# Optimization experiments

Hardware: AMD Instinct MI355X
Metric: run time of the kernel (lower is better)

## Reference

```python
import jax, jax.numpy as jnp
import numpy as np

N_NODES = 100000
N_EDGES = 1600000
HIDDEN = 128
N_FILTERS = 64
CUTOFF = 8.0
BN_EPS = 1e-3  # keras BatchNormalization default epsilon


def setup_inputs() -> dict:
    key = jax.random.key(0)
    ks = jax.random.split(key, 12)
    x = jax.random.normal(ks[0], (N_NODES, HIDDEN), dtype=jnp.float32)
    edge_index = jax.random.randint(ks[1], (2, N_EDGES), 0, N_NODES, dtype=jnp.int32)
    edge_weight = jax.random.uniform(ks[2], (N_EDGES,), dtype=jnp.float32) * CUTOFF
    edge_attr = jax.random.uniform(ks[3], (N_EDGES, 1), dtype=jnp.float32)
    s = 0.05
    # filter_net: Dense(1->64, tanh), Dense(64->64)
    Wf1 = jax.random.normal(ks[4], (1, N_FILTERS), dtype=jnp.float32) * s
    bf1 = jnp.zeros((N_FILTERS,), jnp.float32)
    Wf2 = jax.random.normal(ks[5], (N_FILTERS, N_FILTERS), dtype=jnp.float32) * s
    bf2 = jnp.zeros((N_FILTERS,), jnp.float32)
    # interaction_net: Dense(128->128, softplus), Dense(128->128)
    Wi1 = jax.random.normal(ks[6], (HIDDEN, HIDDEN), dtype=jnp.float32) * s
    bi1 = jnp.zeros((HIDDEN,), jnp.float32)
    Wi2 = jax.random.normal(ks[7], (HIDDEN, HIDDEN), dtype=jnp.float32) * s
    bi2 = jnp.zeros((HIDDEN,), jnp.float32)
    # BatchNormalization (inference: moving stats)
    gamma = jnp.ones((HIDDEN,), jnp.float32)
    beta = jnp.zeros((HIDDEN,), jnp.float32)
    mov_mean = jax.random.normal(ks[8], (HIDDEN,), dtype=jnp.float32) * 0.01
    mov_var = jnp.ones((HIDDEN,), jnp.float32)
    return {"x": x, "edge_index": edge_index, "edge_weight": edge_weight,
            "edge_attr": edge_attr, "Wf1": Wf1, "bf1": bf1, "Wf2": Wf2, "bf2": bf2,
            "Wi1": Wi1, "bi1": bi1, "Wi2": Wi2, "bi2": bi2,
            "gamma": gamma, "beta": beta, "mov_mean": mov_mean, "mov_var": mov_var}


def reference(x, edge_index, edge_weight, edge_attr, Wf1, bf1, Wf2, bf2,
              Wi1, bi1, Wi2, bi2, gamma, beta, mov_mean, mov_var):
    row, col = edge_index[0], edge_index[1]
    # continuous filters with smooth cosine cutoff
    scaled = edge_weight * (2.0 / CUTOFF) - 1.0                    # [E]
    h = jnp.tanh(scaled[:, None] @ Wf1 + bf1)                      # [E, F]
    filters = h @ Wf2 + bf2                                        # [E, F]
    cut = 0.5 * (jnp.cos(edge_weight * jnp.pi / CUTOFF) + 1.0)
    cut = jnp.where(edge_weight <= CUTOFF, cut, 0.0)               # [E]
    filters = filters * cut[:, None]
    # Original: (neighbor[:, None, :] * filters[:, :, None]).sum(axis=1)
    # == neighbor * filters.sum(-1, keepdims) — same math, no [E,F,H] tensor.
    fsum = jnp.sum(filters, axis=-1, keepdims=True)                # [E, 1]
    messages = x[col] * fsum                                       # [E, H]
    agg = jax.ops.segment_sum(messages, row, num_segments=x.shape[0])  # [N, H]
    out = jax.nn.softplus(agg @ Wi1 + bi1) @ Wi2 + bi2             # [N, H]
    # BatchNormalization, inference mode (training=False)
    out = gamma * (out - mov_mean) * jax.lax.rsqrt(mov_var + BN_EPS) + beta
    return out
```

## Files before the change

kernel.cpp:

```cpp
#include <hip/hip_runtime.h>
#include <math.h>

#define HIDDEN 128
#define NFILT 64
#define SCAN_B 1024
#define LUTK 2048

typedef __attribute__((ext_vector_type(8))) short bf16x8;
typedef __attribute__((ext_vector_type(4))) float f32x4;
typedef __attribute__((ext_vector_type(4))) float f32x4v;
typedef __attribute__((ext_vector_type(2))) int i32x2;

__device__ __forceinline__ short f2bf(float f) {
    unsigned u = __float_as_uint(f);
    unsigned r = (u + 0x7fffu + ((u >> 16) & 1u)) >> 16;
    return (short)r;
}
__device__ __forceinline__ float bf2f(unsigned short u) {
    return __uint_as_float(((unsigned)u) << 16);
}

__device__ __forceinline__ float softplus_fast(float v) {
    float e = __builtin_amdgcn_exp2f(v * 1.4426950408889634f);
    float r = 0.69314718055994531f * __builtin_amdgcn_logf(1.0f + e);
    return (v > 80.f) ? v : r;
}

__global__ void wsum_kernel(const float* __restrict__ Wf2, const float* __restrict__ bf2,
                            float* __restrict__ wsum, float* __restrict__ bsum) {
    int j = threadIdx.x;
    float s = 0.f;
    for (int f = 0; f < NFILT; ++f) s += Wf2[j * NFILT + f];
    wsum[j] = s;
    if (j == 0) {
        float b = 0.f;
        for (int f = 0; f < NFILT; ++f) b += bf2[f];
        *bsum = b;
    }
}

__device__ __forceinline__ float edge_coeff(float w,
                                            const float* sW, const float* sB,
                                            const float* sS, float bsum) {
    float s = fmaf(w, 0.25f, -1.0f);
    float acc = bsum;
    #pragma unroll 8
    for (int j = 0; j < NFILT; ++j)
        acc += tanhf(fmaf(s, sW[j], sB[j])) * sS[j];
    float cut = (w <= 8.0f) ? 0.5f * (cosf(w * 0.39269908169872414f) + 1.0f) : 0.0f;
    return acc * cut;
}

__global__ void lut_kernel(const float* __restrict__ Wf1, const float* __restrict__ bf1,
                           const float* __restrict__ wsum, const float* __restrict__ bsum,
                           float* __restrict__ lut) {
    int i = blockIdx.x * 256 + threadIdx.x;
    if (i > LUTK) return;
    float w = 8.0f * (float)i / (float)LUTK;
    lut[i] = edge_coeff(w, Wf1, bf1, wsum, *bsum);
}

__device__ __forceinline__ float lut_eval(const float* sl, float w) {
    float t = w * ((float)LUTK / 8.0f);
    t = fminf(fmaxf(t, 0.f), (float)LUTK);
    int i = (int)t;
    i = min(i, LUTK - 1);
    return fmaf(t - (float)i, sl[i + 1] - sl[i], sl[i]);
}

__global__ void prep_w_kernel(const float* __restrict__ Wi1, const float* __restrict__ Wi2,
                              short* __restrict__ W1T, short* __restrict__ W2T,
                              const float* __restrict__ Wf2, const float* __restrict__ bf2,
                              float* __restrict__ wsum, float* __restrict__ bsum,
                              const float* __restrict__ bi2,
                              const float* __restrict__ gamma, const float* __restrict__ beta,
                              const float* __restrict__ mean, const float* __restrict__ var,
                              float* __restrict__ scf, float* __restrict__ shf,
                              int* __restrict__ zbuf, int zn) {
    int idx = blockIdx.x * 256 + threadIdx.x;
    const float* src = (idx < 16384) ? Wi1 : Wi2;
    short* dst = (idx < 16384) ? W1T : W2T;
    int i = idx & 16383;
    int k = i >> 7, n = i & 127;
    dst[n * HIDDEN + k] = f2bf(src[i]);

    for (int z = idx; z * 4 < zn; z += 32768) {
        if (z * 4 + 3 < zn) *(int4*)&zbuf[z * 4] = make_int4(0, 0, 0, 0);
        else for (int q = z * 4; q < zn; ++q) zbuf[q] = 0;
    }

    if (blockIdx.x == 0 && threadIdx.x < 64) {
        int j = threadIdx.x;
        float s = 0.f;
        for (int f = 0; f < NFILT; ++f) s += Wf2[j * NFILT + f];
        wsum[j] = s;
        if (j == 0) {
            float b = 0.f;
            for (int f = 0; f < NFILT; ++f) b += bf2[f];
            *bsum = b;
        }
    }
    if (blockIdx.x == 1 && threadIdx.x < HIDDEN) {
        int j = threadIdx.x;
        float sc = gamma[j] * rsqrtf(var[j] + 1e-3f);
        scf[j] = sc;
        shf[j] = (bi2[j] - mean[j]) * sc + beta[j];
    }
}

__global__ __launch_bounds__(256) void x2q_count_kernel(
    const float* __restrict__ x, signed char* __restrict__ xq,
    float* __restrict__ xscale, int N16,
    const int* __restrict__ rows, int* __restrict__ deg,
    int* __restrict__ rank, int E) {
    int i = blockIdx.x * 256 + threadIdx.x;
    if (i < E) rank[i] = atomicAdd(&deg[rows[i]], 1);
    if (i < N16) {
        int node = i >> 4, lane = i & 15;
        const float* xp = &x[(size_t)node * HIDDEN + lane * 8];
        const f32x4v v0 = __builtin_nontemporal_load((const f32x4v*)xp);
        const f32x4v v1 = __builtin_nontemporal_load((const f32x4v*)(xp + 4));
        float v[8] = {v0[0], v0[1], v0[2], v0[3], v1[0], v1[1], v1[2], v1[3]};
        float m = 0.f;
        #pragma unroll
        for (int j = 0; j < 8; ++j) m = fmaxf(m, fabsf(v[j]));
        #pragma unroll
        for (int off = 8; off > 0; off >>= 1)
            m = fmaxf(m, __shfl_xor(m, off, 16));
        float si = (m > 0.f) ? 127.f / m : 0.f;
        int q[8];
        #pragma unroll
        for (int j = 0; j < 8; ++j) q[j] = __float2int_rn(v[j] * si);
        int lo = (q[0] & 0xff) | ((q[1] & 0xff) << 8) |
                 ((q[2] & 0xff) << 16) | ((q[3] & 0xff) << 24);
        int hi = (q[4] & 0xff) | ((q[5] & 0xff) << 8) |
                 ((q[6] & 0xff) << 16) | ((q[7] & 0xff) << 24);
        *(int2*)&xq[(size_t)node * HIDDEN + lane * 8] = make_int2(lo, hi);
        if (lane == 0) xscale[node] = m * (1.f / 127.f);
    }
}

__global__ void count_rank_kernel(const int* __restrict__ rows, int* __restrict__ deg,
                                  int* __restrict__ rank, int E) {
    int e = blockIdx.x * blockDim.x + threadIdx.x;
    if (e < E) rank[e] = atomicAdd(&deg[rows[e]], 1);
}

__global__ void count_kernel(const int* __restrict__ rows, int* __restrict__ deg, int E) {
    int e = blockIdx.x * blockDim.x + threadIdx.x;
    if (e < E) atomicAdd(&deg[rows[e]], 1);
}

__global__ __launch_bounds__(SCAN_B) void scan_p1(const int* __restrict__ deg,
                                                  int* __restrict__ bsums, int N) {
    __shared__ int red[SCAN_B];
    int i = blockIdx.x * SCAN_B + threadIdx.x;
    red[threadIdx.x] = (i < N) ? deg[i] : 0;
    __syncthreads();
    for (int off = SCAN_B / 2; off > 0; off >>= 1) {
        if (threadIdx.x < off) red[threadIdx.x] += red[threadIdx.x + off];
        __syncthreads();
    }
    if (threadIdx.x == 0) bsums[blockIdx.x] = red[0];
}

__global__ __launch_bounds__(SCAN_B) void scan_p2(int* __restrict__ bsums, int B) {
    __shared__ int part[SCAN_B];
    int t = threadIdx.x;
    part[t] = (t < B) ? bsums[t] : 0;
    __syncthreads();
    for (int off = 1; off < SCAN_B; off <<= 1) {
        int v = (t >= off) ? part[t - off] : 0;
        __syncthreads();
        part[t] += v;
        __syncthreads();
    }
    if (t < B) bsums[t] = (t == 0) ? 0 : part[t - 1];
}

template <bool WRITE_CURSOR>
__global__ __launch_bounds__(SCAN_B) void scan_p3_t(int* __restrict__ deg,
                                                    const int* __restrict__ bsums,
                                                    int* __restrict__ offs, int N) {
    __shared__ int part[SCAN_B];
    int t = threadIdx.x;
    int i = blockIdx.x * SCAN_B + t;
    int d = (i < N) ? deg[i] : 0;
    part[t] = d;
    __syncthreads();
    for (int off = 1; off < SCAN_B; off <<= 1) {
        int v = (t >= off) ? part[t - off] : 0;
        __syncthreads();
        part[t] += v;
        __syncthreads();
    }
    int pre = bsums[blockIdx.x] + part[t] - d;
    if (i < N) {
        offs[i] = pre;
        if (WRITE_CURSOR) deg[i] = pre;
        if (i == N - 1) offs[N] = pre + d;
    }
}

__global__ __launch_bounds__(256) void fill_rank_q_kernel(
    const int* __restrict__ rows, const int* __restrict__ cols,
    const float* __restrict__ ew, const int* __restrict__ rank,
    const int* __restrict__ offs, const float* __restrict__ xscale,
    const float* __restrict__ lut, int2* __restrict__ epack, int E) {
    __shared__ float sl[LUTK + 1];
    for (int i = threadIdx.x; i <= LUTK; i += 256) sl[i] = lut[i];
    __syncthreads();
    int e = blockIdx.x * 256 + threadIdx.x;
    if (e >= E) return;
    float f = lut_eval(sl, __builtin_nontemporal_load(&ew[e]));
    int r = __builtin_nontemporal_load(&rows[e]);
    int c = __builtin_nontemporal_load(&cols[e]);
    float fs = f * xscale[c];
    int pos = offs[r] + __builtin_nontemporal_load(&rank[e]);
    epack[pos] = make_int2(c, __float_as_int(fs));
}

__global__ __launch_bounds__(256) void fill_rank_kernel(
    const int* __restrict__ rows, const int* __restrict__ cols,
    const float* __restrict__ ew, const int* __restrict__ rank,
    const int* __restrict__ offs, const float* __restrict__ lut,
    int2* __restrict__ epack, int E) {
    __shared__ float sl[LUTK + 1];
    for (int i = threadIdx.x; i <= LUTK; i += 256) sl[i] = lut[i];
    __syncthreads();
    int e = blockIdx.x * 256 + threadIdx.x;
    if (e >= E) return;
    float f = lut_eval(sl, __builtin_nontemporal_load(&ew[e]));
    int pos = offs[__builtin_nontemporal_load(&rows[e])] +
              __builtin_nontemporal_load(&rank[e]);
    epack[pos] = make_int2(__builtin_nontemporal_load(&cols[e]), __float_as_int(f));
}

__global__ __launch_bounds__(256) void fill_cursor_kernel(
    const int* __restrict__ rows, const int* __restrict__ cols,
    const float* __restrict__ ew, int* __restrict__ cursor,
    const float* __restrict__ lut, int2* __restrict__ epack, int E) {
    __shared__ float sl[LUTK + 1];
    for (int i = threadIdx.x; i <= LUTK; i += 256) sl[i] = lut[i];
    __syncthreads();
    int e = blockIdx.x * 256 + threadIdx.x;
    if (e >= E) return;
    float f = lut_eval(sl, ew[e]);
    int pos = atomicAdd(&cursor[rows[e]], 1);
    epack[pos] = make_int2(cols[e], __float_as_int(f));
}

__device__ __forceinline__ void qfma8(int lo, int hi, float f, float* a) {
    a[0] = fmaf((float)((int)(((unsigned)lo) << 24) >> 24), f, a[0]);
    a[1] = fmaf((float)((int)(((unsigned)lo) << 16) >> 24), f, a[1]);
    a[2] = fmaf((float)((int)(((unsigned)lo) << 8) >> 24), f, a[2]);
    a[3] = fmaf((float)(lo >> 24), f, a[3]);
    a[4] = fmaf((float)((int)(((unsigned)hi) << 24) >> 24), f, a[4]);
    a[5] = fmaf((float)((int)(((unsigned)hi) << 16) >> 24), f, a[5]);
    a[6] = fmaf((float)((int)(((unsigned)hi) << 8) >> 24), f, a[6]);
    a[7] = fmaf((float)(hi >> 24), f, a[7]);
}

__device__ __forceinline__ void qfma16(int4 q, float f, float* a) {
    qfma8(q.x, q.y, f, a);
    qfma8(q.z, q.w, f, a + 8);
}

__global__ __launch_bounds__(256) void gather_q8_kernel(const int* __restrict__ offs,
                                                        const int2* __restrict__ epack,
                                                        const signed char* __restrict__ xq,
                                                        short* __restrict__ aggh, int N) {
    int t = threadIdx.x;
    int node = blockIdx.x * 32 + (t >> 3);
    if (node >= N) return;
    int lane = t & 7;
    int s = offs[node], eend = offs[node + 1];
    const signed char* xb = xq + lane * 16;

    float a[16];
    #pragma unroll
    for (int j = 0; j < 16; ++j) a[j] = 0.f;

    int i = s;
    for (; i + 4 <= eend; i += 4) {
        i32x2 p0 = __builtin_nontemporal_load((const i32x2*)&epack[i]);
        i32x2 p1 = __builtin_nontemporal_load((const i32x2*)&epack[i + 1]);
        i32x2 p2 = __builtin_nontemporal_load((const i32x2*)&epack[i + 2]);
        i32x2 p3 = __builtin_nontemporal_load((const i32x2*)&epack[i + 3]);
        int4 q0 = *(const int4*)(xb + (size_t)p0[0] * HIDDEN);
        int4 q1 = *(const int4*)(xb + (size_t)p1[0] * HIDDEN);
        int4 q2 = *(const int4*)(xb + (size_t)p2[0] * HIDDEN);
        int4 q3 = *(const int4*)(xb + (size_t)p3[0] * HIDDEN);
        qfma16(q0, __int_as_float(p0[1]), a);
        qfma16(q1, __int_as_float(p1[1]), a);
        qfma16(q2, __int_as_float(p2[1]), a);
        qfma16(q3, __int_as_float(p3[1]), a);
    }
    for (; i < eend; ++i) {
        i32x2 p = __builtin_nontemporal_load((const i32x2*)&epack[i]);
        int4 q = *(const int4*)(xb + (size_t)p[0] * HIDDEN);
        qfma16(q, __int_as_float(p[1]), a);
    }

    bf16x8 o0, o1;
    #pragma unroll
    for (int j = 0; j < 8; ++j) { o0[j] = f2bf(a[j]); o1[j] = f2bf(a[j + 8]); }
    short* op = &aggh[(size_t)node * HIDDEN + lane * 16];
    *(bf16x8*)op = o0;
    *(bf16x8*)(op + 8) = o1;
}

__global__ __launch_bounds__(256) void gather_kernel(const int* __restrict__ offs,
                                                     const int2* __restrict__ epack,
                                                     const float* __restrict__ x,
                                                     float* __restrict__ agg, int N) {
    int t = threadIdx.x;
    int node = blockIdx.x * 8 + (t >> 5);
    if (node >= N) return;
    int lane = t & 31;
    int s = offs[node], eend = offs[node + 1];
    float4 acc = make_float4(0.f, 0.f, 0.f, 0.f);
    int i = s;
    for (; i + 2 <= eend; i += 2) {
        int2 p0 = epack[i];
        int2 p1 = epack[i + 1];
        float4 x0 = *(const float4*)&x[(size_t)p0.x * HIDDEN + lane * 4];
        float4 x1 = *(const float4*)&x[(size_t)p1.x * HIDDEN + lane * 4];
        float f0 = __int_as_float(p0.y), f1 = __int_as_float(p1.y);
        acc.x = fmaf(x0.x, f0, acc.x); acc.y = fmaf(x0.y, f0, acc.y);
        acc.z = fmaf(x0.z, f0, acc.z); acc.w = fmaf(x0.w, f0, acc.w);
        acc.x = fmaf(x1.x, f1, acc.x); acc.y = fmaf(x1.y, f1, acc.y);
        acc.z = fmaf(x1.z, f1, acc.z); acc.w = fmaf(x1.w, f1, acc.w);
    }
    for (; i < eend; ++i) {
        int2 p = epack[i];
        float f = __int_as_float(p.y);
        const float4 xv = *(const float4*)&x[(size_t)p.x * HIDDEN + lane * 4];
        acc.x = fmaf(xv.x, f, acc.x);
        acc.y = fmaf(xv.y, f, acc.y);
        acc.z = fmaf(xv.z, f, acc.z);
        acc.w = fmaf(xv.w, f, acc.w);
    }
    *(float4*)&agg[(size_t)node * HIDDEN + lane * 4] = acc;
}

#define HROW 136

#define WSWZ(b) ((b) ^ ((((b) >> 8) & 7) << 4))

__global__ __launch_bounds__(512) void mlp_mfma_bf_kernel(
    const short* __restrict__ aggh, float* __restrict__ io,
    const short* __restrict__ W1T, const short* __restrict__ W2T,
    const float* __restrict__ bi1,
    const float* __restrict__ scf, const float* __restrict__ shf,
    int N) {
    __shared__ short wS[HIDDEN * HIDDEN];
    __shared__ short hS[128 * HROW];

    const int t = threadIdx.x;
    const int wave = t >> 6;
    const int lane = t & 63;
    const int quad = lane >> 4;
    const int m16  = lane & 15;
    const int row0 = blockIdx.x * 128 + wave * 16;
    const int arow = row0 + m16;

    const int swzmask = (m16 & 7) << 4;

    bf16x8 w2r[4];
    {
        const bf16x8* w1v = (const bf16x8*)W1T;
        const bf16x8* w2v = (const bf16x8*)W2T;
        bf16x8 w1r[4];
        #pragma unroll
        for (int j = 0; j < 4; ++j) w1r[j] = w1v[t + 512 * j];
        #pragma unroll
        for (int j = 0; j < 4; ++j) w2r[j] = w2v[t + 512 * j];
        #pragma unroll
        for (int j = 0; j < 4; ++j) {
            int b = (t + 512 * j) * 16;
            *(bf16x8*)((char*)wS + WSWZ(b)) = w1r[j];
        }
    }

    float b1v[8];
    #pragma unroll
    for (int ct = 0; ct < 8; ++ct) b1v[ct] = bi1[ct * 16 + m16];

    f32x4 acc[8];
    #pragma unroll
    for (int ct = 0; ct < 8; ++ct) acc[ct] = (f32x4)(0.f);

    __syncthreads();

    #pragma unroll
    for (int ks = 0; ks < 4; ++ks) {
        bf16x8 a;
        if (arow < N) {
            a = *(const bf16x8*)&aggh[(size_t)arow * HIDDEN + ks * 32 + quad * 8];
        } else {
            #pragma unroll
            for (int j = 0; j < 8; ++j) a[j] = 0;
        }
        const char* bbase = (const char*)wS + m16 * 256 + ((ks * 64 + quad * 16) ^ swzmask);
        #pragma unroll
        for (int ct = 0; ct < 8; ++ct) {
            bf16x8 b = *(const bf16x8*)(bbase + ct * 4096);
            acc[ct] = __builtin_amdgcn_mfma_f32_16x16x32_bf16(a, b, acc[ct], 0, 0, 0);
        }
    }

    #pragma unroll
    for (int ct = 0; ct < 8; ++ct) {
        int col = ct * 16 + m16;
        #pragma unroll
        for (int r = 0; r < 4; ++r) {
            int lrow = wave * 16 + quad * 4 + r;
            float h = softplus_fast(acc[ct][r] + b1v[ct]);
            hS[lrow * HROW + col] = f2bf(h);
        }
        acc[ct] = (f32x4)(0.f);
    }
    __syncthreads();

    #pragma unroll
    for (int j = 0; j < 4; ++j) {
        int b = (t + 512 * j) * 16;
        *(bf16x8*)((char*)wS + WSWZ(b)) = w2r[j];
    }
    __syncthreads();

    float scv[8], shv[8];
    #pragma unroll
    for (int ct = 0; ct < 8; ++ct) {
        scv[ct] = scf[ct * 16 + m16];
        shv[ct] = shf[ct * 16 + m16];
    }

    #pragma unroll
    for (int ks = 0; ks < 4; ++ks) {
        bf16x8 a = *(const bf16x8*)&hS[(wave * 16 + m16) * HROW + ks * 32 + quad * 8];
        const char* bbase = (const char*)wS + m16 * 256 + ((ks * 64 + quad * 16) ^ swzmask);
        #pragma unroll
        for (int ct = 0; ct < 8; ++ct) {
            bf16x8 b = *(const bf16x8*)(bbase + ct * 4096);
            acc[ct] = __builtin_amdgcn_mfma_f32_16x16x32_bf16(a, b, acc[ct], 0, 0, 0);
        }
    }

    #pragma unroll
    for (int r = 0; r < 4; ++r) {
        int grow = row0 + quad * 4 + r;
        if (grow < N) {
            float* p = &io[(size_t)grow * HIDDEN + m16];
            #pragma unroll
            for (int ct = 0; ct < 8; ++ct)
                __builtin_nontemporal_store(fmaf(acc[ct][r], scv[ct], shv[ct]), p + ct * 16);
        }
    }
}

__global__ __launch_bounds__(256) void mlp_mfma_kernel(
    float* io,
    const short* __restrict__ W1T, const short* __restrict__ W2T,
    const float* __restrict__ bi1,
    const float* __restrict__ scf, const float* __restrict__ shf,
    int N) {
    __shared__ short hS[64 * HROW];

    const int t = threadIdx.x;
    const int wave = t >> 6;
    const int lane = t & 63;
    const int quad = lane >> 4;
    const int m16  = lane & 15;
    const int row0 = blockIdx.x * 64 + wave * 16;
    const int arow = row0 + m16;

    f32x4 acc[8];
    #pragma unroll
    for (int ct = 0; ct < 8; ++ct) acc[ct] = (f32x4)(0.f);

    #pragma unroll
    for (int ks = 0; ks < 4; ++ks) {
        bf16x8 a;
        if (arow < N) {
            const float* ap = &io[(size_t)arow * HIDDEN + ks * 32 + quad * 8];
            float4 v0 = *(const float4*)ap;
            float4 v1 = *(const float4*)(ap + 4);
            a[0] = f2bf(v0.x); a[1] = f2bf(v0.y); a[2] = f2bf(v0.z); a[3] = f2bf(v0.w);
            a[4] = f2bf(v1.x); a[5] = f2bf(v1.y); a[6] = f2bf(v1.z); a[7] = f2bf(v1.w);
        } else {
            #pragma unroll
            for (int j = 0; j < 8; ++j) a[j] = 0;
        }
        #pragma unroll
        for (int ct = 0; ct < 8; ++ct) {
            bf16x8 b = *(const bf16x8*)&W1T[(ct * 16 + m16) * HIDDEN + ks * 32 + quad * 8];
            acc[ct] = __builtin_amdgcn_mfma_f32_16x16x32_bf16(a, b, acc[ct], 0, 0, 0);
        }
    }

    #pragma unroll
    for (int ct = 0; ct < 8; ++ct) {
        int col = ct * 16 + m16;
        float b1 = bi1[col];
        #pragma unroll
        for (int r = 0; r < 4; ++r) {
            int lrow = wave * 16 + quad * 4 + r;
            float h = softplus_fast(acc[ct][r] + b1);
            hS[lrow * HROW + col] = f2bf(h);
            acc[ct][r] = 0.f;
        }
    }
    __syncthreads();

    #pragma unroll
    for (int ks = 0; ks < 4; ++ks) {
        bf16x8 a = *(const bf16x8*)&hS[(wave * 16 + m16) * HROW + ks * 32 + quad * 8];
        #pragma unroll
        for (int ct = 0; ct < 8; ++ct) {
            bf16x8 b = *(const bf16x8*)&W2T[(ct * 16 + m16) * HIDDEN + ks * 32 + quad * 8];
            acc[ct] = __builtin_amdgcn_mfma_f32_16x16x32_bf16(a, b, acc[ct], 0, 0, 0);
        }
    }

    #pragma unroll
    for (int ct = 0; ct < 8; ++ct) {
        int col = ct * 16 + m16;
        float sc = scf[col], sh = shf[col];
        #pragma unroll
        for (int r = 0; r < 4; ++r) {
            int grow = row0 + quad * 4 + r;
            if (grow < N)
                io[(size_t)grow * HIDDEN + col] = fmaf(acc[ct][r], sc, sh);
        }
    }
}

__global__ void edge_filter_kernel(const float* __restrict__ ew,
                                   const float* __restrict__ Wf1, const float* __restrict__ bf1,
                                   const float* __restrict__ wsum, const float* __restrict__ bsum,
                                   float* __restrict__ fs, int E) {
    __shared__ float sW[NFILT], sB[NFILT], sS[NFILT];
    if (threadIdx.x < NFILT) {
        sW[threadIdx.x] = Wf1[threadIdx.x];
        sB[threadIdx.x] = bf1[threadIdx.x];
        sS[threadIdx.x] = wsum[threadIdx.x];
    }
    __syncthreads();
    int e = blockIdx.x * blockDim.x + threadIdx.x;
    if (e >= E) return;
    fs[e] = edge_coeff(ew[e], sW, sB, sS, *bsum);
}

__global__ void scatter_kernel(const int* __restrict__ rows, const int* __restrict__ cols,
                               const float* __restrict__ x, const float* __restrict__ fs,
                               float* __restrict__ agg, int E) {
    int t = threadIdx.x;
    int e = blockIdx.x * 8 + (t >> 5);
    if (e >= E) return;
    int lane = t & 31;
    int r = rows[e];
    int c = cols[e];
    float f = fs[e];
    const float4 xv = *(const float4*)&x[c * HIDDEN + lane * 4];
    float* dst = &agg[r * HIDDEN + lane * 4];
    atomicAdd(dst + 0, xv.x * f);
    atomicAdd(dst + 1, xv.y * f);
    atomicAdd(dst + 2, xv.z * f);
    atomicAdd(dst + 3, xv.w * f);
}

__global__ __launch_bounds__(256) void mlp_kernel(
    float* __restrict__ io,
    const float* __restrict__ Wi1, const float* __restrict__ bi1,
    const float* __restrict__ Wi2, const float* __restrict__ bi2,
    const float* __restrict__ gamma, const float* __restrict__ beta,
    const float* __restrict__ mean, const float* __restrict__ var,
    int N) {
    __shared__ float As[64 * HIDDEN];
    __shared__ float Wh[64 * HIDDEN];

    const int t = threadIdx.x;
    const int row0 = blockIdx.x * 64;
    const int col4 = (t & 31) * 4;
    const int rgrp = t >> 5;

    #pragma unroll
    for (int i = 0; i < 8; ++i) {
        int f4 = t + 256 * i;
        int r = f4 >> 5, c4 = (f4 & 31) * 4;
        int node = row0 + r;
        float4 v = make_float4(0.f, 0.f, 0.f, 0.f);
        if (node < N) v = *(const float4*)&io[node * HIDDEN + c4];
        *(float4*)&As[r * HIDDEN + c4] = v;
    }

    float acc[8][4];
    #pragma unroll
    for (int r = 0; r < 8; ++r)
        for (int j = 0; j < 4; ++j) acc[r][j] = 0.f;

    for (int kh = 0; kh < 2; ++kh) {
        __syncthreads();
        #pragma unroll
        for (int i = 0; i < 8; ++i) {
            int f4 = t + 256 * i;
            int kr = f4 >> 5, c4 = (f4 & 31) * 4;
            *(float4*)&Wh[kr * HIDDEN + c4] = *(const float4*)&Wi1[(kh * 64 + kr) * HIDDEN + c4];
        }
        __syncthreads();
        for (int k = 0; k < 64; ++k) {
            float4 w = *(const float4*)&Wh[k * HIDDEN + col4];
            #pragma unroll
            for (int r = 0; r < 8; ++r) {
                float a = As[(rgrp + 8 * r) * HIDDEN + kh * 64 + k];
                acc[r][0] = fmaf(a, w.x, acc[r][0]);
                acc[r][1] = fmaf(a, w.y, acc[r][1]);
                acc[r][2] = fmaf(a, w.z, acc[r][2]);
                acc[r][3] = fmaf(a, w.w, acc[r][3]);
            }
        }
    }
    __syncthreads();

    {
        float4 b = *(const float4*)&bi1[col4];
        float bv[4] = {b.x, b.y, b.z, b.w};
        #pragma unroll
        for (int r = 0; r < 8; ++r) {
            float hv[4];
            #pragma unroll
            for (int j = 0; j < 4; ++j) {
                float v = acc[r][j] + bv[j];
                hv[j] = softplus_fast(v);
                acc[r][j] = 0.f;
            }
            *(float4*)&As[(rgrp + 8 * r) * HIDDEN + col4] =
                make_float4(hv[0], hv[1], hv[2], hv[3]);
        }
    }

    for (int kh = 0; kh < 2; ++kh) {
        __syncthreads();
        #pragma unroll
        for (int i = 0; i < 8; ++i) {
            int f4 = t + 256 * i;
            int kr = f4 >> 5, c4 = (f4 & 31) * 4;
            *(float4*)&Wh[kr * HIDDEN + c4] = *(const float4*)&Wi2[(kh * 64 + kr) * HIDDEN + c4];
        }
        __syncthreads();
        for (int k = 0; k < 64; ++k) {
            float4 w = *(const float4*)&Wh[k * HIDDEN + col4];
            #pragma unroll
            for (int r = 0; r < 8; ++r) {
                float a = As[(rgrp + 8 * r) * HIDDEN + kh * 64 + k];
                acc[r][0] = fmaf(a, w.x, acc[r][0]);
                acc[r][1] = fmaf(a, w.y, acc[r][1]);
                acc[r][2] = fmaf(a, w.z, acc[r][2]);
                acc[r][3] = fmaf(a, w.w, acc[r][3]);
            }
        }
    }

    {
        float4 b2 = *(const float4*)&bi2[col4];
        float4 g  = *(const float4*)&gamma[col4];
        float4 be = *(const float4*)&beta[col4];
        float4 mu = *(const float4*)&mean[col4];
        float4 va = *(const float4*)&var[col4];
        float bv[4]  = {b2.x, b2.y, b2.z, b2.w};
        float gv[4]  = {g.x, g.y, g.z, g.w};
        float bev[4] = {be.x, be.y, be.z, be.w};
        float muv[4] = {mu.x, mu.y, mu.z, mu.w};
        float vav[4] = {va.x, va.y, va.z, va.w};
        float sc[4];
        #pragma unroll
        for (int j = 0; j < 4; ++j) sc[j] = gv[j] * rsqrtf(vav[j] + 1e-3f);
        #pragma unroll
        for (int r = 0; r < 8; ++r) {
            int node = row0 + rgrp + 8 * r;
            if (node < N) {
                float o[4];
                #pragma unroll
                for (int j = 0; j < 4; ++j)
                    o[j] = (acc[r][j] + bv[j] - muv[j]) * sc[j] + bev[j];
                *(float4*)&io[node * HIDDEN + col4] = make_float4(o[0], o[1], o[2], o[3]);
            }
        }
    }
}

extern "C" void kernel_launch(void* const* d_in, const int* in_sizes, int n_in,
                              void* d_out, int out_size, void* d_ws, size_t ws_size,
                              hipStream_t stream) {
    const float* x    = (const float*)d_in[0];
    const int*   ei   = (const int*)d_in[1];
    const float* ew   = (const float*)d_in[2];
    const float* Wf1  = (const float*)d_in[4];
    const float* bf1  = (const float*)d_in[5];
    const float* Wf2  = (const float*)d_in[6];
    const float* bf2  = (const float*)d_in[7];
    const float* Wi1  = (const float*)d_in[8];
    const float* bi1  = (const float*)d_in[9];
    const float* Wi2  = (const float*)d_in[10];
    const float* bi2  = (const float*)d_in[11];
    const float* gam  = (const float*)d_in[12];
    const float* bet  = (const float*)d_in[13];
    const float* mmu  = (const float*)d_in[14];
    const float* mva  = (const float*)d_in[15];

    const int N = in_sizes[0] / HIDDEN;
    const int E = in_sizes[2];
    const int* rows = ei;
    const int* cols = ei + E;

    float* io = (float*)d_out;

    const int B = (N + SCAN_B - 1) / SCAN_B;

    char* ws = (char*)d_ws;
    int*   deg    = (int*)ws;
    int*   offs   = deg + N;
    int*   bsums  = offs + N + 1;
    float* wsumv  = (float*)(bsums + B);
    float* bsumv  = wsumv + NFILT;
    float* lut    = bsumv + 1;
    size_t hdr_ints  = (size_t)(2 * N + 1 + B + NFILT + 1 + LUTK + 1);
    size_t epack_off = ((hdr_ints * 4) + 15) & ~(size_t)15;
    int2*  epack  = (int2*)(ws + epack_off);
    size_t wT_off = (epack_off + (size_t)E * sizeof(int2) + 15) & ~(size_t)15;
    short* W1T    = (short*)(ws + wT_off);
    short* W2T    = W1T + HIDDEN * HIDDEN;
    float* scf    = (float*)(W2T + HIDDEN * HIDDEN);
    float* shf    = scf + HIDDEN;
    size_t base_need = wT_off + 2 * HIDDEN * HIDDEN * sizeof(short) + 2 * HIDDEN * sizeof(float);
    size_t rank_off  = (base_need + 15) & ~(size_t)15;
    int*   rank   = (int*)(ws + rank_off);
    size_t rank_need = rank_off + (size_t)E * sizeof(int);
    size_t xq_off    = (rank_need + 15) & ~(size_t)15;
    signed char* xq  = (signed char*)(ws + xq_off);
    size_t xs_off    = (xq_off + (size_t)N * HIDDEN + 15) & ~(size_t)15;
    float* xscale    = (float*)(ws + xs_off);
    size_t ag_off    = (xs_off + (size_t)N * sizeof(float) + 15) & ~(size_t)15;
    short* aggh      = (short*)(ws + ag_off);
    size_t bf_need   = ag_off + (size_t)N * HIDDEN * sizeof(short);

    if (ws_size >= base_need && B <= SCAN_B) {
        const bool use_rank = (ws_size >= rank_need);
        const bool use_bf   = (ws_size >= bf_need);
        if (!use_bf) {
            hipMemsetAsync(deg, 0, (size_t)N * sizeof(int), stream);
        }
        prep_w_kernel<<<128, 256, 0, stream>>>(Wi1, Wi2, W1T, W2T,
                                               Wf2, bf2, wsumv, bsumv,
                                               bi2, gam, bet, mmu, mva, scf, shf,
                                               deg, use_bf ? N : 0);
        lut_kernel<<<(LUTK + 256) / 256, 256, 0, stream>>>(Wf1, bf1, wsumv, bsumv, lut);
        if (use_bf) {
            int N16 = N * 16;
            int work = (N16 > E) ? N16 : E;
            x2q_count_kernel<<<(work + 255) / 256, 256, 0, stream>>>(x, xq, xscale, N16,
                                                                     rows, deg, rank, E);
        } else if (use_rank) {
            count_rank_kernel<<<(E + 255) / 256, 256, 0, stream>>>(rows, deg, rank, E);
        } else {
            count_kernel<<<(E + 255) / 256, 256, 0, stream>>>(rows, deg, E);
        }
        scan_p1<<<B, SCAN_B, 0, stream>>>(deg, bsums, N);
        scan_p2<<<1, SCAN_B, 0, stream>>>(bsums, B);
        if (use_bf) {
            scan_p3_t<false><<<B, SCAN_B, 0, stream>>>(deg, bsums, offs, N);
            fill_rank_q_kernel<<<(E + 255) / 256, 256, 0, stream>>>(rows, cols, ew, rank,
                                                                    offs, xscale, lut,
                                                                    epack, E);
            gather_q8_kernel<<<(N + 31) / 32, 256, 0, stream>>>(offs, epack, xq, aggh, N);
            mlp_mfma_bf_kernel<<<(N + 127) / 128, 512, 0, stream>>>(aggh, io, W1T, W2T,
                                                                    bi1, scf, shf, N);
        } else if (use_rank) {
            scan_p3_t<false><<<B, SCAN_B, 0, stream>>>(deg, bsums, offs, N);
            fill_rank_kernel<<<(E + 255) / 256, 256, 0, stream>>>(rows, cols, ew, rank,
                                                                  offs, lut, epack, E);
            gather_kernel<<<(N + 7) / 8, 256, 0, stream>>>(offs, epack, x, io, N);
            mlp_mfma_kernel<<<(N + 63) / 64, 256, 0, stream>>>(io, W1T, W2T, bi1, scf, shf, N);
        } else {
            scan_p3_t<true><<<B, SCAN_B, 0, stream>>>(deg, bsums, offs, N);
            fill_cursor_kernel<<<(E + 255) / 256, 256, 0, stream>>>(rows, cols, ew, deg,
                                                                    lut, epack, E);
            gather_kernel<<<(N + 7) / 8, 256, 0, stream>>>(offs, epack, x, io, N);
            mlp_mfma_kernel<<<(N + 63) / 64, 256, 0, stream>>>(io, W1T, W2T, bi1, scf, shf, N);
        }
    } else {
        float* fs = (float*)d_ws;
        float* w2 = fs + E;
        float* b2 = w2 + NFILT;
        hipMemsetAsync(d_out, 0, (size_t)out_size * sizeof(float), stream);
        wsum_kernel<<<1, 64, 0, stream>>>(Wf2, bf2, w2, b2);
        edge_filter_kernel<<<(E + 255) / 256, 256, 0, stream>>>(ew, Wf1, bf1, w2, b2, fs, E);
        scatter_kernel<<<(E + 7) / 8, 256, 0, stream>>>(rows, cols, x, fs, io, E);
        mlp_kernel<<<(N + 63) / 64, 256, 0, stream>>>(io, Wi1, bi1, Wi2, bi2,
                                                      gam, bet, mmu, mva, N);
    }
}
```

Before: 342.2 us.

## Fuse count, scan and fill into one persistent kernel with grid barriers

Replaces the separate quantize/count, three-pass scan, and fill kernels with a single persistent kernel of 196 blocks that separates its phases with atomic-counter grid barriers. The LUT construction is folded into prep_w_kernel, which also zeroes the barrier counter. This removes several kernel launches and their inter-kernel gaps. In exchange it relies on all 196 blocks being co-resident for the spin barriers, and the grid-stride loops run at lower parallelism than the original launches.

```diff
diff --git a/kernel.cpp b/kernel.cpp
--- a/kernel.cpp
+++ b/kernel.cpp
@@ -5,6 +5,8 @@
 #define NFILT 64
 #define SCAN_B 1024
 #define LUTK 2048
+#define NBLK 196
+#define BBS  512
 
 typedef __attribute__((ext_vector_type(8))) short bf16x8;
 typedef __attribute__((ext_vector_type(4))) float f32x4;
@@ -24,6 +26,21 @@
     float e = __builtin_amdgcn_exp2f(v * 1.4426950408889634f);
     float r = 0.69314718055994531f * __builtin_amdgcn_logf(1.0f + e);
     return (v > 80.f) ? v : r;
+}
+
+__device__ __forceinline__ void gridbar(int* cnt, int phase) {
+    __syncthreads();
+    if (threadIdx.x == 0) {
+        __threadfence();
+        atomicAdd(cnt, 1);
+        int need = NBLK * phase;
+        while (__hip_atomic_load(cnt, __ATOMIC_ACQUIRE,
+                                 __HIP_MEMORY_SCOPE_AGENT) < need) {
+            __builtin_amdgcn_s_sleep(8);
+        }
+        __threadfence();
+    }
+    __syncthreads();
 }
 
 __global__ void wsum_kernel(const float* __restrict__ Wf2, const float* __restrict__ bf2,
@@ -51,15 +68,6 @@
     return acc * cut;
 }
 
-__global__ void lut_kernel(const float* __restrict__ Wf1, const float* __restrict__ bf1,
-                           const float* __restrict__ wsum, const float* __restrict__ bsum,
-                           float* __restrict__ lut) {
-    int i = blockIdx.x * 256 + threadIdx.x;
-    if (i > LUTK) return;
-    float w = 8.0f * (float)i / (float)LUTK;
-    lut[i] = edge_coeff(w, Wf1, bf1, wsum, *bsum);
-}
-
 __device__ __forceinline__ float lut_eval(const float* sl, float w) {
     float t = w * ((float)LUTK / 8.0f);
     t = fminf(fmaxf(t, 0.f), (float)LUTK);
@@ -76,7 +84,12 @@
                               const float* __restrict__ gamma, const float* __restrict__ beta,
                               const float* __restrict__ mean, const float* __restrict__ var,
                               float* __restrict__ scf, float* __restrict__ shf,
+                              const float* __restrict__ Wf1, const float* __restrict__ bf1,
+                              float* __restrict__ lut,
                               int* __restrict__ zbuf, int zn) {
+    __shared__ float sW[NFILT], sB[NFILT], sS[NFILT];
+    __shared__ float sbsum;
+
     int idx = blockIdx.x * 256 + threadIdx.x;
     const float* src = (idx < 16384) ? Wi1 : Wi2;
     short* dst = (idx < 16384) ? W1T : W2T;
@@ -106,37 +119,120 @@
         scf[j] = sc;
         shf[j] = (bi2[j] - mean[j]) * sc + beta[j];
     }
-}
-
-__global__ __launch_bounds__(256) void x2q_count_kernel(
+    if (blockIdx.x >= 2 && blockIdx.x <= 10) {
+        if (threadIdx.x < NFILT) {
+            int j = threadIdx.x;
+            float s = 0.f;
+            for (int f = 0; f < NFILT; ++f) s += Wf2[j * NFILT + f];
+            sS[j] = s;
+            sW[j] = Wf1[j];
+            sB[j] = bf1[j];
+        }
+        if (threadIdx.x == 0) {
+            float b = 0.f;
+            for (int f = 0; f < NFILT; ++f) b += bf2[f];
+            sbsum = b;
+        }
+        __syncthreads();
+        int li = (blockIdx.x - 2) * 256 + threadIdx.x;
+        if (li <= LUTK) {
+            float w = 8.0f * (float)li / (float)LUTK;
+            lut[li] = edge_coeff(w, sW, sB, sS, sbsum);
+        }
+    }
+}
+
+__global__ __launch_bounds__(BBS) void build_kernel(
     const float* __restrict__ x, signed char* __restrict__ xq,
-    float* __restrict__ xscale, int N16,
-    const int* __restrict__ rows, int* __restrict__ deg,
-    int* __restrict__ rank, int E) {
-    int i = blockIdx.x * 256 + threadIdx.x;
-    if (i < E) rank[i] = atomicAdd(&deg[rows[i]], 1);
-    if (i < N16) {
-        int node = i >> 4, lane = i & 15;
-        const float* xp = &x[(size_t)node * HIDDEN + lane * 8];
-        const f32x4v v0 = __builtin_nontemporal_load((const f32x4v*)xp);
-        const f32x4v v1 = __builtin_nontemporal_load((const f32x4v*)(xp + 4));
-        float v[8] = {v0[0], v0[1], v0[2], v0[3], v1[0], v1[1], v1[2], v1[3]};
-        float m = 0.f;
-        #pragma unroll
-        for (int j = 0; j < 8; ++j) m = fmaxf(m, fabsf(v[j]));
-        #pragma unroll
-        for (int off = 8; off > 0; off >>= 1)
-            m = fmaxf(m, __shfl_xor(m, off, 16));
-        float si = (m > 0.f) ? 127.f / m : 0.f;
-        int q[8];
-        #pragma unroll
-        for (int j = 0; j < 8; ++j) q[j] = __float2int_rn(v[j] * si);
-        int lo = (q[0] & 0xff) | ((q[1] & 0xff) << 8) |
-                 ((q[2] & 0xff) << 16) | ((q[3] & 0xff) << 24);
-        int hi = (q[4] & 0xff) | ((q[5] & 0xff) << 8) |
-                 ((q[6] & 0xff) << 16) | ((q[7] & 0xff) << 24);
-        *(int2*)&xq[(size_t)node * HIDDEN + lane * 8] = make_int2(lo, hi);
-        if (lane == 0) xscale[node] = m * (1.f / 127.f);
+    float* __restrict__ xscale,
+    const int* __restrict__ rows, const int* __restrict__ cols,
+    const float* __restrict__ ew,
+    int* __restrict__ deg, int* __restrict__ rank,
+    int* __restrict__ bsums, int* __restrict__ offs,
+    int* __restrict__ barcnt, const float* __restrict__ lut,
+    int2* __restrict__ epack, int E, int N, int N16) {
+    __shared__ float sl[LUTK + 1];
+    __shared__ int part[BBS];
+    __shared__ int bs2[256];
+
+    const int t = threadIdx.x;
+    const int bk = blockIdx.x;
+    const int gid0 = bk * BBS + t;
+    const int GSZ = NBLK * BBS;
+
+    for (int i = t; i <= LUTK; i += BBS) sl[i] = lut[i];
+
+    int work = (N16 > E) ? N16 : E;
+    for (int i = gid0; i < work; i += GSZ) {
+        if (i < E) rank[i] = atomicAdd(&deg[rows[i]], 1);
+        if (i < N16) {
+            int node = i >> 4, lane = i & 15;
+            const float* xp = &x[(size_t)node * HIDDEN + lane * 8];
+            const f32x4v v0 = __builtin_nontemporal_load((const f32x4v*)xp);
+            const f32x4v v1 = __builtin_nontemporal_load((const f32x4v*)(xp + 4));
+            float v[8] = {v0[0], v0[1], v0[2], v0[3], v1[0], v1[1], v1[2], v1[3]};
+            float m = 0.f;
+            #pragma unroll
+            for (int j = 0; j < 8; ++j) m = fmaxf(m, fabsf(v[j]));
+            #pragma unroll
+            for (int off = 8; off > 0; off >>= 1)
+                m = fmaxf(m, __shfl_xor(m, off, 16));
+            float si = (m > 0.f) ? 127.f / m : 0.f;
+            int q[8];
+            #pragma unroll
+            for (int j = 0; j < 8; ++j) q[j] = __float2int_rn(v[j] * si);
+            int lo = (q[0] & 0xff) | ((q[1] & 0xff) << 8) |
+                     ((q[2] & 0xff) << 16) | ((q[3] & 0xff) << 24);
+            int hi = (q[4] & 0xff) | ((q[5] & 0xff) << 8) |
+                     ((q[6] & 0xff) << 16) | ((q[7] & 0xff) << 24);
+            *(int2*)&xq[(size_t)node * HIDDEN + lane * 8] = make_int2(lo, hi);
+            if (lane == 0) xscale[node] = m * (1.f / 127.f);
+        }
+    }
+    gridbar(barcnt, 1);
+
+    int j = gid0;
+    int d = (j < N) ? deg[j] : 0;
+    part[t] = d;
+    __syncthreads();
+    for (int off = 1; off < BBS; off <<= 1) {
+        int v = (t >= off) ? part[t - off] : 0;
+        __syncthreads();
+        part[t] += v;
+        __syncthreads();
+    }
+    int incl = part[t];
+    if (t == 0) bsums[bk] = part[BBS - 1];
+    gridbar(barcnt, 2);
+
+    if (bk == 0) {
+        int v = (t < NBLK) ? bsums[t] : 0;
+        if (t < 256) bs2[t] = v;
+        __syncthreads();
+        for (int off = 1; off < 256; off <<= 1) {
+            int v2 = (t >= off && t < 256) ? bs2[t - off] : 0;
+            __syncthreads();
+            if (t < 256) bs2[t] += v2;
+            __syncthreads();
+        }
+        if (t < NBLK) bsums[t] = (t == 0) ? 0 : bs2[t - 1];
+    }
+    gridbar(barcnt, 3);
+
+    int base = bsums[bk];
+    if (j < N) {
+        offs[j] = base + incl - d;
+        if (j == N - 1) offs[N] = base + incl;
+    }
+    gridbar(barcnt, 4);
+
+    for (int e = gid0; e < E; e += GSZ) {
+        float f = lut_eval(sl, __builtin_nontemporal_load(&ew[e]));
+        int r = __builtin_nontemporal_load(&rows[e]);
+        int c = __builtin_nontemporal_load(&cols[e]);
+        float fs = f * xscale[c];
+        int pos = offs[r] + __builtin_nontemporal_load(&rank[e]);
+        epack[pos] = make_int2(c, __float_as_int(fs));
     }
 }
 
@@ -200,24 +296,6 @@
         if (WRITE_CURSOR) deg[i] = pre;
         if (i == N - 1) offs[N] = pre + d;
     }
-}
-
-__global__ __launch_bounds__(256) void fill_rank_q_kernel(
-    const int* __restrict__ rows, const int* __restrict__ cols,
-    const float* __restrict__ ew, const int* __restrict__ rank,
-    const int* __restrict__ offs, const float* __restrict__ xscale,
-    const float* __restrict__ lut, int2* __restrict__ epack, int E) {
-    __shared__ float sl[LUTK + 1];
-    for (int i = threadIdx.x; i <= LUTK; i += 256) sl[i] = lut[i];
-    __syncthreads();
-    int e = blockIdx.x * 256 + threadIdx.x;
-    if (e >= E) return;
-    float f = lut_eval(sl, __builtin_nontemporal_load(&ew[e]));
-    int r = __builtin_nontemporal_load(&rows[e]);
-    int c = __builtin_nontemporal_load(&cols[e]);
-    float fs = f * xscale[c];
-    int pos = offs[r] + __builtin_nontemporal_load(&rank[e]);
-    epack[pos] = make_int2(c, __float_as_int(fs));
 }
 
 __global__ __launch_bounds__(256) void fill_rank_kernel(
@@ -345,7 +423,6 @@
 }
 
 #define HROW 136
-
 #define WSWZ(b) ((b) ^ ((((b) >> 8) & 7) << 4))
 
 __global__ __launch_bounds__(512) void mlp_mfma_bf_kernel(
@@ -721,12 +798,13 @@
 
     char* ws = (char*)d_ws;
     int*   deg    = (int*)ws;
-    int*   offs   = deg + N;
+    int*   barcnt = deg + N;
+    int*   offs   = barcnt + 4;
     int*   bsums  = offs + N + 1;
-    float* wsumv  = (float*)(bsums + B);
+    float* wsumv  = (float*)(bsums + 256);
     float* bsumv  = wsumv + NFILT;
     float* lut    = bsumv + 1;
-    size_t hdr_ints  = (size_t)(2 * N + 1 + B + NFILT + 1 + LUTK + 1);
+    size_t hdr_ints  = (size_t)(N + 4 + N + 1 + 256 + NFILT + 1 + LUTK + 1);
     size_t epack_off = ((hdr_ints * 4) + 15) & ~(size_t)15;
     int2*  epack  = (int2*)(ws + epack_off);
     size_t wT_off = (epack_off + (size_t)E * sizeof(int2) + 15) & ~(size_t)15;
@@ -749,41 +827,36 @@
     if (ws_size >= base_need && B <= SCAN_B) {
         const bool use_rank = (ws_size >= rank_need);
         const bool use_bf   = (ws_size >= bf_need);
-        if (!use_bf) {
+        const bool use_mega = use_bf && (N <= NBLK * BBS);
+        if (!use_mega) {
             hipMemsetAsync(deg, 0, (size_t)N * sizeof(int), stream);
         }
         prep_w_kernel<<<128, 256, 0, stream>>>(Wi1, Wi2, W1T, W2T,
                                                Wf2, bf2, wsumv, bsumv,
                                                bi2, gam, bet, mmu, mva, scf, shf,
-                                               deg, use_bf ? N : 0);
-        lut_kernel<<<(LUTK + 256) / 256, 256, 0, stream>>>(Wf1, bf1, wsumv, bsumv, lut);
-        if (use_bf) {
+                                               Wf1, bf1, lut,
+                                               deg, use_mega ? N + 4 : 0);
+        if (use_mega) {
             int N16 = N * 16;
-            int work = (N16 > E) ? N16 : E;
-            x2q_count_kernel<<<(work + 255) / 256, 256, 0, stream>>>(x, xq, xscale, N16,
-                                                                     rows, deg, rank, E);
-        } else if (use_rank) {
-            count_rank_kernel<<<(E + 255) / 256, 256, 0, stream>>>(rows, deg, rank, E);
-        } else {
-            count_kernel<<<(E + 255) / 256, 256, 0, stream>>>(rows, deg, E);
-        }
-        scan_p1<<<B, SCAN_B, 0, stream>>>(deg, bsums, N);
-        scan_p2<<<1, SCAN_B, 0, stream>>>(bsums, B);
-        if (use_bf) {
-            scan_p3_t<false><<<B, SCAN_B, 0, stream>>>(deg, bsums, offs, N);
-            fill_rank_q_kernel<<<(E + 255) / 256, 256, 0, stream>>>(rows, cols, ew, rank,
-                                                                    offs, xscale, lut,
-                                                                    epack, E);
+            build_kernel<<<NBLK, BBS, 0, stream>>>(x, xq, xscale, rows, cols, ew,
+                                                   deg, rank, bsums, offs, barcnt,
+                                                   lut, epack, E, N, N16);
             gather_q8_kernel<<<(N + 31) / 32, 256, 0, stream>>>(offs, epack, xq, aggh, N);
             mlp_mfma_bf_kernel<<<(N + 127) / 128, 512, 0, stream>>>(aggh, io, W1T, W2T,
                                                                     bi1, scf, shf, N);
         } else if (use_rank) {
+            count_rank_kernel<<<(E + 255) / 256, 256, 0, stream>>>(rows, deg, rank, E);
+            scan_p1<<<B, SCAN_B, 0, stream>>>(deg, bsums, N);
+            scan_p2<<<1, SCAN_B, 0, stream>>>(bsums, B);
             scan_p3_t<false><<<B, SCAN_B, 0, stream>>>(deg, bsums, offs, N);
             fill_rank_kernel<<<(E + 255) / 256, 256, 0, stream>>>(rows, cols, ew, rank,
                                                                   offs, lut, epack, E);
             gather_kernel<<<(N + 7) / 8, 256, 0, stream>>>(offs, epack, x, io, N);
             mlp_mfma_kernel<<<(N + 63) / 64, 256, 0, stream>>>(io, W1T, W2T, bi1, scf, shf, N);
         } else {
+            count_kernel<<<(E + 255) / 256, 256, 0, stream>>>(rows, deg, E);
+            scan_p1<<<B, SCAN_B, 0, stream>>>(deg, bsums, N);
+            scan_p2<<<1, SCAN_B, 0, stream>>>(bsums, B);
             scan_p3_t<true><<<B, SCAN_B, 0, stream>>>(deg, bsums, offs, N);
             fill_cursor_kernel<<<(E + 255) / 256, 256, 0, stream>>>(rows, cols, ew, deg,
                                                                     lut, epack, E);
```

Result: slower. 408.8 us (+19.4%).

## Replace three-pass scan with single-pass decoupled lookback and fold LUT into prep

Applied to the files above, without the earlier changes.

The three-kernel prefix scan (block sums, scan of sums, add-back) on the quantized path becomes one decoupled-lookback kernel with ticket-ordered blocks and flag/value state words. LUT construction moves into extra blocks of prep_w_kernel, dropping another launch. The goal is to cut launch count and inter-kernel gaps on a pipeline of small kernels. The lookback spins across blocks, and the fast path now also requires even N and a bounded scan-block count.

```diff
diff --git a/kernel.cpp b/kernel.cpp
--- a/kernel.cpp
+++ b/kernel.cpp
@@ -5,6 +5,8 @@
 #define NFILT 64
 #define SCAN_B 1024
 #define LUTK 2048
+#define SC_EPB 4096
+#define SC_MAXNB 1024
 
 typedef __attribute__((ext_vector_type(8))) short bf16x8;
 typedef __attribute__((ext_vector_type(4))) float f32x4;
@@ -51,15 +53,6 @@
     return acc * cut;
 }
 
-__global__ void lut_kernel(const float* __restrict__ Wf1, const float* __restrict__ bf1,
-                           const float* __restrict__ wsum, const float* __restrict__ bsum,
-                           float* __restrict__ lut) {
-    int i = blockIdx.x * 256 + threadIdx.x;
-    if (i > LUTK) return;
-    float w = 8.0f * (float)i / (float)LUTK;
-    lut[i] = edge_coeff(w, Wf1, bf1, wsum, *bsum);
-}
-
 __device__ __forceinline__ float lut_eval(const float* sl, float w) {
     float t = w * ((float)LUTK / 8.0f);
     t = fminf(fmaxf(t, 0.f), (float)LUTK);
@@ -76,7 +69,12 @@
                               const float* __restrict__ gamma, const float* __restrict__ beta,
                               const float* __restrict__ mean, const float* __restrict__ var,
                               float* __restrict__ scf, float* __restrict__ shf,
+                              const float* __restrict__ Wf1, const float* __restrict__ bf1,
+                              float* __restrict__ lut,
                               int* __restrict__ zbuf, int zn) {
+    __shared__ float sW[NFILT], sB[NFILT], sS[NFILT];
+    __shared__ float sbsum;
+
     int idx = blockIdx.x * 256 + threadIdx.x;
     const float* src = (idx < 16384) ? Wi1 : Wi2;
     short* dst = (idx < 16384) ? W1T : W2T;
@@ -105,6 +103,27 @@
         float sc = gamma[j] * rsqrtf(var[j] + 1e-3f);
         scf[j] = sc;
         shf[j] = (bi2[j] - mean[j]) * sc + beta[j];
+    }
+    if (blockIdx.x >= 2 && blockIdx.x <= 10) {
+        if (threadIdx.x < NFILT) {
+            int j = threadIdx.x;
+            float s = 0.f;
+            for (int f = 0; f < NFILT; ++f) s += Wf2[j * NFILT + f];
+            sS[j] = s;
+            sW[j] = Wf1[j];
+            sB[j] = bf1[j];
+        }
+        if (threadIdx.x == 0) {
+            float b = 0.f;
+            for (int f = 0; f < NFILT; ++f) b += bf2[f];
+            sbsum = b;
+        }
+        __syncthreads();
+        int li = (blockIdx.x - 2) * 256 + threadIdx.x;
+        if (li <= LUTK) {
+            float w = 8.0f * (float)li / (float)LUTK;
+            lut[li] = edge_coeff(w, sW, sB, sS, sbsum);
+        }
     }
 }
 
@@ -138,6 +157,86 @@
         *(int2*)&xq[(size_t)node * HIDDEN + lane * 8] = make_int2(lo, hi);
         if (lane == 0) xscale[node] = m * (1.f / 127.f);
     }
+}
+
+#define FL_AGG (1LL << 62)
+#define FL_PFX (2LL << 62)
+#define FL_MSK (3LL << 62)
+
+__global__ __launch_bounds__(1024) void scan_lookback_kernel(
+    const int* __restrict__ deg, int* __restrict__ offs,
+    int* __restrict__ ticket, long long* __restrict__ state, int N) {
+    __shared__ int sbid;
+    __shared__ int spart[1024];
+    __shared__ int sprev;
+
+    const int t = threadIdx.x;
+    if (t == 0) sbid = atomicAdd(ticket, 1);
+    __syncthreads();
+    const int bid = sbid;
+    const int base = bid * SC_EPB;
+    const int i0 = base + t * 4;
+
+    int v0 = 0, v1 = 0, v2 = 0, v3 = 0;
+    if (i0 + 3 < N) {
+        int4 dv = *(const int4*)&deg[i0];
+        v0 = dv.x; v1 = dv.y; v2 = dv.z; v3 = dv.w;
+    } else {
+        if (i0 + 0 < N) v0 = deg[i0 + 0];
+        if (i0 + 1 < N) v1 = deg[i0 + 1];
+        if (i0 + 2 < N) v2 = deg[i0 + 2];
+        if (i0 + 3 < N) v3 = deg[i0 + 3];
+    }
+    int s0 = v0, s1 = s0 + v1, s2 = s1 + v2, s3 = s2 + v3;
+
+    spart[t] = s3;
+    __syncthreads();
+    for (int off = 1; off < 1024; off <<= 1) {
+        int vv = (t >= off) ? spart[t - off] : 0;
+        __syncthreads();
+        spart[t] += vv;
+        __syncthreads();
+    }
+    int incl = spart[t];
+    int btot = spart[1023];
+
+    if (t == 0) {
+        if (bid == 0) {
+            __hip_atomic_store(&state[0], FL_PFX | (long long)btot,
+                               __ATOMIC_RELEASE, __HIP_MEMORY_SCOPE_AGENT);
+            sprev = 0;
+        } else {
+            __hip_atomic_store(&state[bid], FL_AGG | (long long)btot,
+                               __ATOMIC_RELEASE, __HIP_MEMORY_SCOPE_AGENT);
+            long long run = 0;
+            int j = bid - 1;
+            while (j >= 0) {
+                long long s;
+                do {
+                    s = __hip_atomic_load(&state[j], __ATOMIC_ACQUIRE,
+                                          __HIP_MEMORY_SCOPE_AGENT);
+                    if ((s & FL_MSK) == 0) __builtin_amdgcn_s_sleep(2);
+                } while ((s & FL_MSK) == 0);
+                run += (s & ~FL_MSK);
+                if ((s & FL_MSK) == FL_PFX) break;
+                --j;
+            }
+            sprev = (int)run;
+            __hip_atomic_store(&state[bid], FL_PFX | (run + (long long)btot),
+                               __ATOMIC_RELEASE, __HIP_MEMORY_SCOPE_AGENT);
+        }
+    }
+    __syncthreads();
+    const int prev = sprev;
+
+    int ebase = prev + incl - s3;
+    if (i0 + 0 < N) offs[i0 + 0] = ebase;
+    if (i0 + 1 < N) offs[i0 + 1] = ebase + s0;
+    if (i0 + 2 < N) offs[i0 + 2] = ebase + s1;
+    if (i0 + 3 < N) offs[i0 + 3] = ebase + s2;
+    if (N - 1 >= i0 && N - 1 < i0 + 4) offs[N] = ebase + s3 -
+        ((N - 1 == i0 + 0) ? (s3 - s0) : (N - 1 == i0 + 1) ? (s3 - s1)
+         : (N - 1 == i0 + 2) ? (s3 - s2) : 0);
 }
 
 __global__ void count_rank_kernel(const int* __restrict__ rows, int* __restrict__ deg,
@@ -345,7 +444,6 @@
 }
 
 #define HROW 136
-
 #define WSWZ(b) ((b) ^ ((((b) >> 8) & 7) << 4))
 
 __global__ __launch_bounds__(512) void mlp_mfma_bf_kernel(
@@ -718,15 +816,18 @@
     float* io = (float*)d_out;
 
     const int B = (N + SCAN_B - 1) / SCAN_B;
+    const int NB_SCAN = (N + SC_EPB - 1) / SC_EPB;
 
     char* ws = (char*)d_ws;
     int*   deg    = (int*)ws;
-    int*   offs   = deg + N;
+    int*   ticket = deg + N;
+    long long* state = (long long*)(ticket + 2);
+    int*   offs   = (int*)(state + SC_MAXNB);
     int*   bsums  = offs + N + 1;
-    float* wsumv  = (float*)(bsums + B);
+    float* wsumv  = (float*)(bsums + SCAN_B);
     float* bsumv  = wsumv + NFILT;
     float* lut    = bsumv + 1;
-    size_t hdr_ints  = (size_t)(2 * N + 1 + B + NFILT + 1 + LUTK + 1);
+    size_t hdr_ints  = (size_t)(N + 2 + 2 * SC_MAXNB + N + 1 + SCAN_B + NFILT + 1 + LUTK + 1);
     size_t epack_off = ((hdr_ints * 4) + 15) & ~(size_t)15;
     int2*  epack  = (int2*)(ws + epack_off);
     size_t wT_off = (epack_off + (size_t)E * sizeof(int2) + 15) & ~(size_t)15;
@@ -748,29 +849,23 @@
 
     if (ws_size >= base_need && B <= SCAN_B) {
         const bool use_rank = (ws_size >= rank_need);
-        const bool use_bf   = (ws_size >= bf_need);
+        const bool use_bf   = (ws_size >= bf_need) && (NB_SCAN <= SC_MAXNB) &&
+                              ((N & 1) == 0);
         if (!use_bf) {
             hipMemsetAsync(deg, 0, (size_t)N * sizeof(int), stream);
         }
         prep_w_kernel<<<128, 256, 0, stream>>>(Wi1, Wi2, W1T, W2T,
                                                Wf2, bf2, wsumv, bsumv,
                                                bi2, gam, bet, mmu, mva, scf, shf,
-                                               deg, use_bf ? N : 0);
-        lut_kernel<<<(LUTK + 256) / 256, 256, 0, stream>>>(Wf1, bf1, wsumv, bsumv, lut);
+                                               Wf1, bf1, lut,
+                                               deg, use_bf ? N + 2 + 2 * SC_MAXNB : 0);
         if (use_bf) {
             int N16 = N * 16;
             int work = (N16 > E) ? N16 : E;
             x2q_count_kernel<<<(work + 255) / 256, 256, 0, stream>>>(x, xq, xscale, N16,
                                                                      rows, deg, rank, E);
-        } else if (use_rank) {
-            count_rank_kernel<<<(E + 255) / 256, 256, 0, stream>>>(rows, deg, rank, E);
-        } else {
-            count_kernel<<<(E + 255) / 256, 256, 0, stream>>>(rows, deg, E);
-        }
-        scan_p1<<<B, SCAN_B, 0, stream>>>(deg, bsums, N);
-        scan_p2<<<1, SCAN_B, 0, stream>>>(bsums, B);
-        if (use_bf) {
-            scan_p3_t<false><<<B, SCAN_B, 0, stream>>>(deg, bsums, offs, N);
+            scan_lookback_kernel<<<NB_SCAN, 1024, 0, stream>>>(deg, offs, ticket,
+                                                               state, N);
             fill_rank_q_kernel<<<(E + 255) / 256, 256, 0, stream>>>(rows, cols, ew, rank,
                                                                     offs, xscale, lut,
                                                                     epack, E);
@@ -778,12 +873,18 @@
             mlp_mfma_bf_kernel<<<(N + 127) / 128, 512, 0, stream>>>(aggh, io, W1T, W2T,
                                                                     bi1, scf, shf, N);
         } else if (use_rank) {
+            count_rank_kernel<<<(E + 255) / 256, 256, 0, stream>>>(rows, deg, rank, E);
+            scan_p1<<<B, SCAN_B, 0, stream>>>(deg, bsums, N);
+            scan_p2<<<1, SCAN_B, 0, stream>>>(bsums, B);
             scan_p3_t<false><<<B, SCAN_B, 0, stream>>>(deg, bsums, offs, N);
             fill_rank_kernel<<<(E + 255) / 256, 256, 0, stream>>>(rows, cols, ew, rank,
                                                                   offs, lut, epack, E);
             gather_kernel<<<(N + 7) / 8, 256, 0, stream>>>(offs, epack, x, io, N);
             mlp_mfma_kernel<<<(N + 63) / 64, 256, 0, stream>>>(io, W1T, W2T, bi1, scf, shf, N);
         } else {
+            count_kernel<<<(E + 255) / 256, 256, 0, stream>>>(rows, deg, E);
+            scan_p1<<<B, SCAN_B, 0, stream>>>(deg, bsums, N);
+            scan_p2<<<1, SCAN_B, 0, stream>>>(bsums, B);
             scan_p3_t<true><<<B, SCAN_B, 0, stream>>>(deg, bsums, offs, N);
             fill_cursor_kernel<<<(E + 255) / 256, 256, 0, stream>>>(rows, cols, ew, deg,
                                                                     lut, epack, E);
```

Result: no change. 343.7 us (+0.4%).
